# Kernel tuning notes

Hardware: AMD Instinct MI355X
Metric: run time of the kernel (lower is better)

## Reference

```python
import jax, jax.numpy as jnp
import numpy as np


def setup_inputs() -> dict:
    key = jax.random.key(0)
    k1, k2, k3 = jax.random.split(key, 3)
    B, L, S, H, E, D = 2, 512, 512, 8, 32, 64
    queries = jax.random.normal(k1, (B, L, H, E), dtype=jnp.float32)
    keys = jax.random.normal(k2, (B, S, H, E), dtype=jnp.float32)
    values = jax.random.normal(k3, (B, S, H, D), dtype=jnp.float32)
    v = jnp.ones((E,), dtype=jnp.float32)
    attn_mask_add = jnp.zeros((L, S), dtype=jnp.float32)
    key_lengths_add = jnp.zeros((B, S), dtype=jnp.float32)
    return {
        "queries": queries,
        "keys": keys,
        "values": values,
        "v": v,
        "attn_mask_add": attn_mask_add,
        "key_lengths_add": key_lengths_add,
    }


def reference(queries, keys, values, v, attn_mask_add, key_lengths_add):
    # Additive (Bahdanau) attention.
    # queries: (B,L,H,E), keys: (B,S,H,E), values: (B,S,H,D)
    # Broadcast add -> tanh -> contract with v: (B,L,S,H,E) -> (B,H,L,S)
    feat = jnp.tanh(queries[:, :, None, :, :] + keys[:, None, :, :, :])  # (B,L,S,H,E)
    scores = jnp.einsum("blshe,e->bhls", feat, v)  # (B,H,L,S)
    scores = scores + attn_mask_add[None, None, :, :]          # (L,S) attn mask
    scores = scores + key_lengths_add[:, None, None, :]        # (B,S) key-length mask
    A = jax.nn.softmax(scores, axis=-1)  # (B,H,L,S); dropout is identity (p=0 / eval)
    V = jnp.einsum("bhls,bshd->blhd", A, values)  # (B,L,H,D)
    return V
```

## Files before the change

### kernel.cpp

```cpp
#include <hip/hip_runtime.h>


#define BB 2
#define LL 512
#define SS 512
#define HH 8
#define EE 32
#define DD 64
#define TS 64
#define NT (SS / TS)

#define WS_EK_OFF 0
#define WS_EQ_OFF (2u * 1024u * 1024u)
#define WS_VT_OFF (4u * 1024u * 1024u)

typedef __attribute__((ext_vector_type(8))) short bf16x8;
typedef __attribute__((ext_vector_type(4))) float f32x4;
typedef __attribute__((ext_vector_type(4))) unsigned u32x4;

__device__ __forceinline__ unsigned short f2bf(float f) {
    unsigned u = __float_as_uint(f);
    u += 0x7FFFu + ((u >> 16) & 1u);
    return (unsigned short)(u >> 16);
}
__device__ __forceinline__ float fast_exp2(float x) {
#if __has_builtin(__builtin_amdgcn_exp2f)
    return __builtin_amdgcn_exp2f(x);
#else
    return exp2f(x);
#endif
}
__device__ __forceinline__ float fast_rcp(float x) {
    return __builtin_amdgcn_rcpf(x);
}

#define SCV 2.885390081777927f

__global__ __launch_bounds__(256) void prep_kernel(
    const float* __restrict__ q, const float* __restrict__ k,
    const float* __restrict__ vals, float* __restrict__ ws)
{
    unsigned gid = blockIdx.x * 256 + threadIdx.x;
    if (gid < 65536u) {
        unsigned i  = gid;
        unsigned u  = i & 63u;
        unsigned e4 = (i >> 6) & 7u;
        unsigned t  = (i >> 9) & 7u;
        unsigned h  = (i >> 12) & 7u;
        unsigned b  = i >> 15;
        unsigned s  = t * 64u + (u ^ e4);
        float4 kv = *(const float4*)(k + (((size_t)b * SS + s) * HH + h) * EE + e4 * 4);
        float4 ev = make_float4(fast_exp2(SCV * kv.x), fast_exp2(SCV * kv.y),
                                fast_exp2(SCV * kv.z), fast_exp2(SCV * kv.w));
        ((float4*)(ws + WS_EK_OFF / 4))[i] = ev;
    } else if (gid < 131072u) {
        unsigned i = gid - 65536u;
        float4 qv = ((const float4*)q)[i];
        float4 ev = make_float4(fast_exp2(SCV * qv.x), fast_exp2(SCV * qv.y),
                                fast_exp2(SCV * qv.z), fast_exp2(SCV * qv.w));
        ((float4*)(ws + WS_EQ_OFF / 4))[i] = ev;
    } else {
        unsigned p   = gid - 131072u;
        unsigned sp8 = p & 63u;
        unsigned d   = (p >> 6) & 63u;
        unsigned h   = (p >> 12) & 7u;
        unsigned b   = p >> 15;
        unsigned s0  = sp8 * 8u;
        const float* vb = vals + (((size_t)b * SS + s0) * HH + h) * DD + d;
        u32x4 pk;
        #pragma unroll
        for (int j = 0; j < 4; j++) {
            float f0 = vb[(size_t)(2 * j) * (HH * DD)];
            float f1 = vb[(size_t)(2 * j + 1) * (HH * DD)];
            pk[j] = (unsigned)f2bf(f0) | ((unsigned)f2bf(f1) << 16);
        }
        u32x4* vt4 = (u32x4*)((char*)ws + WS_VT_OFF);
        vt4[((((size_t)b * HH + h) * DD + d) * SS + s0) / 8] = pk;
    }
}

__global__ __launch_bounds__(256) void addattn_kernel(
    const float* __restrict__ ws_ekf,
    const float* __restrict__ ws_eqf,
    const unsigned short* __restrict__ ws_vt,
    const float* __restrict__ vvec,
    const float* __restrict__ mask,
    const float* __restrict__ klen,
    float* __restrict__ out)
{
    __shared__ float4 sk[2][EE / 4][TS];
    __shared__ unsigned short sAb[4][SS];

    const int tid  = threadIdx.x;
    const int w    = tid >> 6;
    const int lane = tid & 63;
    const int bh   = blockIdx.x >> 7;
    const int lblk = blockIdx.x & 127;
    const int b    = bh >> 3;
    const int h    = bh & 7;
    const int l    = lblk * 4 + w;

    float4 eq[EE / 4];
    {
        const float4* qrow =
            (const float4*)(ws_eqf + (((size_t)b * LL + l) * HH + h) * EE);
        #pragma unroll
        for (int e4 = 0; e4 < EE / 4; e4++) eq[e4] = qrow[e4];
    }
    float4 v2[EE / 4];
    {
        const float4* vr = (const float4*)vvec;
        #pragma unroll
        for (int i = 0; i < EE / 4; i++) {
            float4 t = vr[i];
            v2[i] = make_float4(-2.f * t.x, -2.f * t.y, -2.f * t.z, -2.f * t.w);
        }
    }

    const float4* ektiles =
        (const float4*)ws_ekf + (size_t)(b * HH + h) * (NT * 8 * TS);
    {
        float4 p0 = ektiles[tid];
        float4 p1 = ektiles[tid + 256];
        float4* dst = (float4*)sk[0];
        dst[tid] = p0;
        dst[tid + 256] = p1;
    }
    __syncthreads();

    float sc[NT];
    for (int t = 0; t < NT; t++) {
        float4 n0, n1;
        if (t < NT - 1) {
            const float4* src = ektiles + (size_t)(t + 1) * (8 * TS);
            n0 = src[tid];
            n1 = src[tid + 256];
        }
        const int buf = t & 1;
        {
            float a0 = 0.f, a1 = 0.f, a2 = 0.f, a3 = 0.f;
            #pragma unroll
            for (int e4 = 0; e4 < EE / 4; e4++) {
                float4 kv = sk[buf][e4][lane ^ e4];
                float4 ev = eq[e4];
                float4 vv = v2[e4];
                a0 = __builtin_fmaf(vv.x, fast_rcp(__builtin_fmaf(ev.x, kv.x, 1.f)), a0);
                a1 = __builtin_fmaf(vv.y, fast_rcp(__builtin_fmaf(ev.y, kv.y, 1.f)), a1);
                a2 = __builtin_fmaf(vv.z, fast_rcp(__builtin_fmaf(ev.z, kv.z, 1.f)), a2);
                a3 = __builtin_fmaf(vv.w, fast_rcp(__builtin_fmaf(ev.w, kv.w, 1.f)), a3);
            }
            sc[t] = (a0 + a1) + (a2 + a3);
        }
        if (t < NT - 1) {
            float4* dst = (float4*)sk[buf ^ 1];
            dst[tid] = n0;
            dst[tid + 256] = n1;
        }
        __syncthreads();
    }

    {
        const float* mrow = mask + (size_t)l * SS;
        const float* kl   = klen + (size_t)b * SS;
        float mx = -1e30f;
        #pragma unroll
        for (int i = 0; i < SS / 64; i++) {
            int s = lane + i * 64;
            sc[i] += mrow[s] + kl[s];
            mx = fmaxf(mx, sc[i]);
        }
        #pragma unroll
        for (int off = 1; off < 64; off <<= 1) mx = fmaxf(mx, __shfl_xor(mx, off, 64));
        float ssum = 0.f;
        #pragma unroll
        for (int i = 0; i < SS / 64; i++) {
            sc[i] = __expf(sc[i] - mx);
            ssum += sc[i];
        }
        #pragma unroll
        for (int off = 1; off < 64; off <<= 1) ssum += __shfl_xor(ssum, off, 64);
        float inv = fast_rcp(ssum);
        const int fsw = (w * 5) & 7;
        #pragma unroll
        for (int i = 0; i < SS / 64; i++) {
            int col = lane + i * 64;
            int pos = (((col >> 3) ^ fsw) << 3) | (col & 7);
            sAb[w][pos] = f2bf(sc[i] * inv);
        }
    }
    __syncthreads();

    const int am  = lane & 15;
    const int qd  = lane >> 4;
    const int dof = w * 16 + am;
    const int fam = (am * 5) & 7;
    const unsigned short* vt =
        ws_vt + (((size_t)b * HH + h) * DD + dof) * SS + qd * 8;
    f32x4 acc = {0.f, 0.f, 0.f, 0.f};
    bf16x8 bcur = *(const bf16x8*)vt;
    for (int c = 0; c < SS / 32; c++) {
        bf16x8 bnxt = bcur;
        if (c < SS / 32 - 1) bnxt = *(const bf16x8*)(vt + (c + 1) * 32);
        bf16x8 af = {0, 0, 0, 0, 0, 0, 0, 0};
        if (am < 4)
            af = *(const bf16x8*)&sAb[am][((c * 4 + qd) ^ fam) << 3];
        acc = __builtin_amdgcn_mfma_f32_16x16x32_bf16(af, bcur, acc, 0, 0, 0);
        bcur = bnxt;
    }
    if (qd == 0) {
        float* orow = out + (((size_t)b * LL + lblk * 4) * HH + h) * DD + dof;
        #pragma unroll
        for (int r = 0; r < 4; r++)
            orow[(size_t)r * (HH * DD)] = acc[r];
    }
}

extern "C" void kernel_launch(void* const* d_in, const int* in_sizes, int n_in,
                              void* d_out, int out_size, void* d_ws, size_t ws_size,
                              hipStream_t stream) {
    const float* q    = (const float*)d_in[0];
    const float* k    = (const float*)d_in[1];
    const float* vals = (const float*)d_in[2];
    const float* vvec = (const float*)d_in[3];
    const float* mask = (const float*)d_in[4];
    const float* klen = (const float*)d_in[5];
    float* outp = (float*)d_out;

    float* ws = (float*)d_ws;
    prep_kernel<<<dim3(768), dim3(256), 0, stream>>>(q, k, vals, ws);

    const float* ws_ekf = (const float*)((char*)d_ws + WS_EK_OFF);
    const float* ws_eqf = (const float*)((char*)d_ws + WS_EQ_OFF);
    const unsigned short* ws_vt = (const unsigned short*)((char*)d_ws + WS_VT_OFF);
    addattn_kernel<<<dim3(BB * HH * (LL / 4)), dim3(256), 0, stream>>>(
        ws_ekf, ws_eqf, ws_vt, vvec, mask, klen, outp);
}
```

Baseline: 97.39 us.

## Read exp(key) tiles directly from global memory instead of LDS double-buffering

```diff
diff --git a/kernel.cpp b/kernel.cpp
--- a/kernel.cpp
+++ b/kernel.cpp
@@ -7,8 +7,6 @@
 #define HH 8
 #define EE 32
 #define DD 64
-#define TS 64
-#define NT (SS / TS)
 
 #define WS_EK_OFF 0
 #define WS_EQ_OFF (2u * 1024u * 1024u)
@@ -43,12 +41,10 @@
     unsigned gid = blockIdx.x * 256 + threadIdx.x;
     if (gid < 65536u) {
         unsigned i  = gid;
-        unsigned u  = i & 63u;
-        unsigned e4 = (i >> 6) & 7u;
-        unsigned t  = (i >> 9) & 7u;
+        unsigned s  = i & 511u;
+        unsigned e4 = (i >> 9) & 7u;
         unsigned h  = (i >> 12) & 7u;
         unsigned b  = i >> 15;
-        unsigned s  = t * 64u + (u ^ e4);
         float4 kv = *(const float4*)(k + (((size_t)b * SS + s) * HH + h) * EE + e4 * 4);
         float4 ev = make_float4(fast_exp2(SCV * kv.x), fast_exp2(SCV * kv.y),
                                 fast_exp2(SCV * kv.z), fast_exp2(SCV * kv.w));
@@ -88,7 +84,6 @@
     const float* __restrict__ klen,
     float* __restrict__ out)
 {
-    __shared__ float4 sk[2][EE / 4][TS];
     __shared__ unsigned short sAb[4][SS];
 
     const int tid  = threadIdx.x;
@@ -117,46 +112,22 @@
         }
     }
 
-    const float4* ektiles =
-        (const float4*)ws_ekf + (size_t)(b * HH + h) * (NT * 8 * TS);
-    {
-        float4 p0 = ektiles[tid];
-        float4 p1 = ektiles[tid + 256];
-        float4* dst = (float4*)sk[0];
-        dst[tid] = p0;
-        dst[tid + 256] = p1;
-    }
-    __syncthreads();
-
-    float sc[NT];
-    for (int t = 0; t < NT; t++) {
-        float4 n0, n1;
-        if (t < NT - 1) {
-            const float4* src = ektiles + (size_t)(t + 1) * (8 * TS);
-            n0 = src[tid];
-            n1 = src[tid + 256];
-        }
-        const int buf = t & 1;
-        {
-            float a0 = 0.f, a1 = 0.f, a2 = 0.f, a3 = 0.f;
-            #pragma unroll
-            for (int e4 = 0; e4 < EE / 4; e4++) {
-                float4 kv = sk[buf][e4][lane ^ e4];
-                float4 ev = eq[e4];
-                float4 vv = v2[e4];
-                a0 = __builtin_fmaf(vv.x, fast_rcp(__builtin_fmaf(ev.x, kv.x, 1.f)), a0);
-                a1 = __builtin_fmaf(vv.y, fast_rcp(__builtin_fmaf(ev.y, kv.y, 1.f)), a1);
-                a2 = __builtin_fmaf(vv.z, fast_rcp(__builtin_fmaf(ev.z, kv.z, 1.f)), a2);
-                a3 = __builtin_fmaf(vv.w, fast_rcp(__builtin_fmaf(ev.w, kv.w, 1.f)), a3);
-            }
-            sc[t] = (a0 + a1) + (a2 + a3);
-        }
-        if (t < NT - 1) {
-            float4* dst = (float4*)sk[buf ^ 1];
-            dst[tid] = n0;
-            dst[tid + 256] = n1;
-        }
-        __syncthreads();
+    float sc[SS / 64];
+    const float4* ekp = (const float4*)ws_ekf + (size_t)(b * HH + h) * (8 * SS);
+    for (int i = 0; i < SS / 64; i++) {
+        int s = lane + i * 64;
+        float a0 = 0.f, a1 = 0.f, a2 = 0.f, a3 = 0.f;
+        #pragma unroll
+        for (int e4 = 0; e4 < EE / 4; e4++) {
+            float4 kv = ekp[e4 * SS + s];
+            float4 ev = eq[e4];
+            float4 vv = v2[e4];
+            a0 = __builtin_fmaf(vv.x, fast_rcp(__builtin_fmaf(ev.x, kv.x, 1.f)), a0);
+            a1 = __builtin_fmaf(vv.y, fast_rcp(__builtin_fmaf(ev.y, kv.y, 1.f)), a1);
+            a2 = __builtin_fmaf(vv.z, fast_rcp(__builtin_fmaf(ev.z, kv.z, 1.f)), a2);
+            a3 = __builtin_fmaf(vv.w, fast_rcp(__builtin_fmaf(ev.w, kv.w, 1.f)), a3);
+        }
+        sc[i] = (a0 + a1) + (a2 + a3);
     }
 
     {
```

Result: slower. 127.9 us (+31.3%).
